# Optimization experiments

Hardware: AMD Instinct MI355X
Metric: run time of the kernel (lower is better)

The kernel has to match this reference:

```python
import jax, jax.numpy as jnp
import numpy as np

B, N, C = 1, 2048, 1024
H, D = 16, 64          # num_heads, head_dim
S = 8                  # number of frames; tokens per frame = N // S
NEG_INF = jnp.float32(-1e30)  # stand-in for -inf, numerically safe under jit


def setup_inputs() -> dict:
    key = jax.random.key(0)
    ks = jax.random.split(key, 8)
    x = jax.random.normal(ks[0], (B, N, C), dtype=jnp.float32)
    # tokens grouped contiguously by frame (sorted frame ids)
    frame_ids = jnp.repeat(jnp.arange(S, dtype=jnp.int32), N // S)
    is_hub = jax.random.bernoulli(ks[1], 0.05, (N,))
    adj = jax.random.bernoulli(ks[2], 0.25, (S, S))
    adj = adj.at[jnp.arange(S), jnp.arange(S)].set(True)  # frames always see self
    frame_bias = jax.random.normal(ks[3], (S, S), dtype=jnp.float32) * 0.1
    Wqkv = jax.random.normal(ks[4], (C, 3 * C), dtype=jnp.float32) * 0.02
    bqkv = jnp.zeros((3 * C,), dtype=jnp.float32)
    Wproj = jax.random.normal(ks[5], (C, C), dtype=jnp.float32) * 0.02
    bproj = jnp.zeros((C,), dtype=jnp.float32)
    return {"x": x, "frame_ids": frame_ids, "is_hub": is_hub, "adj": adj,
            "frame_bias": frame_bias, "Wqkv": Wqkv, "bqkv": bqkv,
            "Wproj": Wproj, "bproj": bproj}


def reference(x, frame_ids, is_hub, adj, frame_bias, Wqkv, bqkv, Wproj, bproj):
    # qkv projection: (B,N,3C) -> (3,B,H,N,D)
    qkv = (x @ Wqkv + bqkv).reshape(B, N, 3, H, D).transpose(2, 0, 3, 1, 4)
    q, k, v = qkv[0], qkv[1], qkv[2]

    # flex_attention: scores scaled by 1/sqrt(D) BEFORE score_mod
    scores = jnp.einsum("bhnd,bhmd->bhnm", q, k) * (D ** -0.5)

    # score_mod, vectorized over all (qi,kj) pairs:
    fi = frame_ids                                   # (N,)
    allow = adj[fi][:, fi]                           # (N,N) frame adjacency per token pair
    diff_frame = fi[:, None] != fi[None, :]
    hub_block = diff_frame & (is_hub[:, None] | is_hub[None, :])
    allow = allow & ~hub_block                       # mask_hub_tokens=True
    bias = frame_bias[fi][:, fi]                     # soft_mask=True: add frame-level bias

    scores = jnp.where(allow, scores + bias, NEG_INF)  # broadcast over (b,h)
    attn = jax.nn.softmax(scores, axis=-1)
    out = jnp.einsum("bhnm,bhmd->bhnd", attn, v)
    out = out.transpose(0, 2, 1, 3).reshape(B, N, C)
    return out @ Wproj + bproj
```

## Files before the change

### kernel.cpp

```cpp
#include <hip/hip_runtime.h>

#define NTOK 2048
#define CDIM 1024
#define NHEAD 16
#define HDIM 64
#define NFRM 8
#define FTOK 256

typedef unsigned short ushort;
typedef __attribute__((ext_vector_type(8))) short short8;
typedef __attribute__((ext_vector_type(8))) ushort ushort8;
typedef __attribute__((ext_vector_type(4))) ushort ushort4v;
typedef __attribute__((ext_vector_type(4))) float floatx4;

__device__ __forceinline__ ushort f2bf(float f) {
    unsigned int u = __float_as_uint(f);
    return (ushort)((u + 0x7fffu + ((u >> 16) & 1u)) >> 16);
}

__device__ __forceinline__ void gload_lds16(const void* g, void* l) {
    __builtin_amdgcn_global_load_lds(
        (const __attribute__((address_space(1))) unsigned int*)(uintptr_t)g,
        (__attribute__((address_space(3))) unsigned int*)(unsigned int)(uintptr_t)l,
        16, 0, 0);
}

__global__ __launch_bounds__(256)
void convx_kernel(const float* __restrict__ x, ushort* __restrict__ xb, int n4)
{
    int i = blockIdx.x * 256 + threadIdx.x;
    if (i < n4) {
        float4 f = ((const float4*)x)[i];
        ushort4v o = { f2bf(f.x), f2bf(f.y), f2bf(f.z), f2bf(f.w) };
        ((ushort4v*)xb)[i] = o;
    }
}

__global__ __launch_bounds__(256)
void wtrans_kernel(const float* __restrict__ W, ushort* __restrict__ WT, int K, int N)
{
    __shared__ ushort LT[64][72];
    const int t = threadIdx.x;
    const int k0 = blockIdx.y * 64, n0 = blockIdx.x * 64;
    const int kr = t >> 4, nc = t & 15;
#pragma unroll
    for (int i = 0; i < 4; ++i) {
        int k = kr + i * 16;
        float4 w4 = *(const float4*)(W + (size_t)(k0 + k) * N + n0 + nc * 4);
        LT[nc*4+0][k] = f2bf(w4.x);
        LT[nc*4+1][k] = f2bf(w4.y);
        LT[nc*4+2][k] = f2bf(w4.z);
        LT[nc*4+3][k] = f2bf(w4.w);
    }
    __syncthreads();
    const int n = t >> 2;
#pragma unroll
    for (int half = 0; half < 2; ++half) {
        int kc = (t & 3) + 4 * half;
        ushort8 v = *(const ushort8*)&LT[n][kc * 8];
        *(ushort8*)(WT + (size_t)(n0 + n) * K + k0 + kc * 8) = v;
    }
}

__global__ __launch_bounds__(256)
void vtrans_kernel(const ushort* __restrict__ v, ushort* __restrict__ vT)
{
    __shared__ ushort LT[64][72];
    const int t = threadIdx.x, h = blockIdx.y, n0 = blockIdx.x * 64;
    {
        const int tok = t >> 2;
#pragma unroll
        for (int half = 0; half < 2; ++half) {
            int dc = (t & 3) + 4 * half;
            ushort8 v8 = *(const ushort8*)(v + ((size_t)h * NTOK + n0 + tok) * HDIM + dc * 8);
#pragma unroll
            for (int j = 0; j < 8; ++j) LT[dc*8 + j][tok] = v8[j];
        }
    }
    __syncthreads();
    {
        const int d = t >> 2;
#pragma unroll
        for (int half = 0; half < 2; ++half) {
            int tc = (t & 3) + 4 * half;
            ushort8 o8 = *(const ushort8*)&LT[d][tc * 8];
            *(ushort8*)(vT + ((size_t)h * HDIM + d) * NTOK + n0 + tc * 8) = o8;
        }
    }
}

__global__ __launch_bounds__(256)
void gemm_bt_kernel(const ushort* __restrict__ A, const ushort* __restrict__ BT,
                    const float* __restrict__ bias, void* __restrict__ out,
                    int M, int N, int K, int mode)
{
    __shared__ ushort As[2][128 * 32];
    __shared__ ushort Bs[2][128 * 32];

    const int t = threadIdx.x;
    const int wave = t >> 6, lane = t & 63;
    const int quad = lane >> 4, l15 = lane & 15;
    const int row0 = blockIdx.y * 128, col0 = blockIdx.x * 128;
    const int wm = (wave >> 1) * 64, wn = (wave & 1) * 64;

    const int sr = lane >> 2;
    const int sc = (lane & 3) * 8;
    const int r0 = wave * 32;

    floatx4 acc[4][4];
#pragma unroll
    for (int i = 0; i < 4; ++i)
#pragma unroll
        for (int j = 0; j < 4; ++j) acc[i][j] = (floatx4){0.f, 0.f, 0.f, 0.f};

    gload_lds16(A  + (size_t)(row0 + r0      + sr) * K + sc, &As[0][ r0       * 32]);
    gload_lds16(A  + (size_t)(row0 + r0 + 16 + sr) * K + sc, &As[0][(r0 + 16) * 32]);
    gload_lds16(BT + (size_t)(col0 + r0      + sr) * K + sc, &Bs[0][ r0       * 32]);
    gload_lds16(BT + (size_t)(col0 + r0 + 16 + sr) * K + sc, &Bs[0][(r0 + 16) * 32]);

    const int nk = K >> 5;
    for (int ki = 0; ki < nk; ++ki) {
        __syncthreads();
        if (ki + 1 < nk) {
            const int kn = (ki + 1) << 5;
            const int b = (ki + 1) & 1;
            gload_lds16(A  + (size_t)(row0 + r0      + sr) * K + kn + sc, &As[b][ r0       * 32]);
            gload_lds16(A  + (size_t)(row0 + r0 + 16 + sr) * K + kn + sc, &As[b][(r0 + 16) * 32]);
            gload_lds16(BT + (size_t)(col0 + r0      + sr) * K + kn + sc, &Bs[b][ r0       * 32]);
            gload_lds16(BT + (size_t)(col0 + r0 + 16 + sr) * K + kn + sc, &Bs[b][(r0 + 16) * 32]);
        }
        const ushort* as = As[ki & 1];
        const ushort* bs = Bs[ki & 1];

        short8 af[4], bfr[4];
#pragma unroll
        for (int i = 0; i < 4; ++i)
            af[i] = *(const short8*)&as[(wm + i * 16 + l15) * 32 + quad * 8];
#pragma unroll
        for (int j = 0; j < 4; ++j)
            bfr[j] = *(const short8*)&bs[(wn + j * 16 + l15) * 32 + quad * 8];
#pragma unroll
        for (int i = 0; i < 4; ++i)
#pragma unroll
            for (int j = 0; j < 4; ++j)
                acc[i][j] = __builtin_amdgcn_mfma_f32_16x16x32_bf16(af[i], bfr[j], acc[i][j], 0, 0, 0);
    }

    if (mode == 0) {
        float* outf = (float*)out;
#pragma unroll
        for (int j = 0; j < 4; ++j) {
            int col = col0 + wn + j * 16 + l15;
            float bb = bias[col];
#pragma unroll
            for (int i = 0; i < 4; ++i) {
                int rowb = row0 + wm + i * 16 + quad * 4;
#pragma unroll
                for (int r = 0; r < 4; ++r)
                    outf[(size_t)(rowb + r) * N + col] = acc[i][j][r] + bb;
            }
        }
    } else {
        ushort* outb = (ushort*)out;
#pragma unroll
        for (int j = 0; j < 4; ++j) {
            int col = col0 + wn + j * 16 + l15;
            float bb = bias[col];
            int part = col >> 10, hh = (col >> 6) & 15, d = col & 63;
            ushort* dst = outb + ((size_t)(part * NHEAD + hh) * NTOK) * HDIM + d;
#pragma unroll
            for (int i = 0; i < 4; ++i) {
                int rowb = row0 + wm + i * 16 + quad * 4;
#pragma unroll
                for (int r = 0; r < 4; ++r)
                    dst[(size_t)(rowb + r) * HDIM] = f2bf(acc[i][j][r] + bb);
            }
        }
    }
}

__global__ __launch_bounds__(256)
void attn_mfma_kernel(const ushort* __restrict__ qkvb,
                      const ushort* __restrict__ vTb,
                      const int* __restrict__ frame_ids,
                      const int* __restrict__ is_hub,
                      const int* __restrict__ adj,
                      const float* __restrict__ frame_bias,
                      ushort* __restrict__ attnb)
{
    __shared__ ushort Qs[64 * 64];
    __shared__ ushort Ks[2][64 * 64];
    __shared__ ushort VTs[2][64 * 64];
    __shared__ ushort Ps[4][16 * 72];

    const int t = threadIdx.x;
    const int wave = t >> 6, lane = t & 63;
    const int quad = lane >> 4, l15 = lane & 15;
    const int h = blockIdx.y, q0 = blockIdx.x * 64;

    const ushort* Qg = qkvb + ((size_t)h * NTOK) * HDIM;
    const ushort* Kg = qkvb + ((size_t)(NHEAD + h) * NTOK) * HDIM;
    const ushort* Vg = vTb + ((size_t)h * HDIM) * NTOK;

    const int sr = lane >> 3;
    const int sc = (lane & 7) * 8;
    const int r0s = wave * 16;

    const int fq = frame_ids[q0];
    unsigned vpack = 0; int nv = 0;
#pragma unroll
    for (int f = 0; f < NFRM; ++f)
        if (adj[fq * NFRM + f]) { vpack |= (unsigned)f << (3 * nv); ++nv; }
    const int ntot = nv * 4;

    {
        gload_lds16(Qg + (size_t)(q0 + r0s     + sr) * HDIM + sc, &Qs[ r0s      * 64]);
        gload_lds16(Qg + (size_t)(q0 + r0s + 8 + sr) * HDIM + sc, &Qs[(r0s + 8) * 64]);
        const int k0 = (int)(vpack & 7u) * FTOK;
        gload_lds16(Kg + (size_t)(k0 + r0s     + sr) * HDIM + sc, &Ks[0][ r0s      * 64]);
        gload_lds16(Kg + (size_t)(k0 + r0s + 8 + sr) * HDIM + sc, &Ks[0][(r0s + 8) * 64]);
        gload_lds16(Vg + (size_t)(r0s     + sr) * NTOK + k0 + sc, &VTs[0][ r0s      * 64]);
        gload_lds16(Vg + (size_t)(r0s + 8 + sr) * NTOK + k0 + sc, &VTs[0][(r0s + 8) * 64]);
    }

    int qh[4];
#pragma unroll
    for (int r = 0; r < 4; ++r) qh[r] = is_hub[q0 + wave * 16 + quad * 4 + r];

    float mcur[4], lcur[4];
    floatx4 oacc[4];
#pragma unroll
    for (int r = 0; r < 4; ++r) { mcur[r] = -3.0e38f; lcur[r] = 0.0f; }
#pragma unroll
    for (int dt = 0; dt < 4; ++dt) oacc[dt] = (floatx4){0.f, 0.f, 0.f, 0.f};

    short8 aq0, aq1;

    for (int vt = 0; vt < ntot; ++vt) {
        const int fj = (int)((vpack >> (3 * (vt >> 2))) & 7u);
        const int k0 = fj * FTOK + (vt & 3) * 64;

        __syncthreads();

        if (vt == 0) {
            aq0 = *(const short8*)&Qs[(wave * 16 + l15) * 64 + quad * 8];
            aq1 = *(const short8*)&Qs[(wave * 16 + l15) * 64 + 32 + quad * 8];
        }
        if (vt + 1 < ntot) {
            const int fn = (int)((vpack >> (3 * ((vt + 1) >> 2))) & 7u);
            const int kn = fn * FTOK + ((vt + 1) & 3) * 64;
            const int b = (vt + 1) & 1;
            gload_lds16(Kg + (size_t)(kn + r0s     + sr) * HDIM + sc, &Ks[b][ r0s      * 64]);
            gload_lds16(Kg + (size_t)(kn + r0s + 8 + sr) * HDIM + sc, &Ks[b][(r0s + 8) * 64]);
            gload_lds16(Vg + (size_t)(r0s     + sr) * NTOK + kn + sc, &VTs[b][ r0s      * 64]);
            gload_lds16(Vg + (size_t)(r0s + 8 + sr) * NTOK + kn + sc, &VTs[b][(r0s + 8) * 64]);
        }

        int kh[4];
#pragma unroll
        for (int nt = 0; nt < 4; ++nt) kh[nt] = is_hub[k0 + nt * 16 + l15];
        const float fb = frame_bias[fq * NFRM + fj];
        const bool same = (fj == fq);

        const ushort* ks = Ks[vt & 1];
        const ushort* vs = VTs[vt & 1];

        floatx4 s[4];
#pragma unroll
        for (int nt = 0; nt < 4; ++nt) s[nt] = (floatx4){0.f, 0.f, 0.f, 0.f};
#pragma unroll
        for (int nt = 0; nt < 4; ++nt) {
            short8 bk0 = *(const short8*)&ks[(nt * 16 + l15) * 64 + quad * 8];
            short8 bk1 = *(const short8*)&ks[(nt * 16 + l15) * 64 + 32 + quad * 8];
            s[nt] = __builtin_amdgcn_mfma_f32_16x16x32_bf16(aq0, bk0, s[nt], 0, 0, 0);
            s[nt] = __builtin_amdgcn_mfma_f32_16x16x32_bf16(aq1, bk1, s[nt], 0, 0, 0);
        }

        float alpha[4];
#pragma unroll
        for (int r = 0; r < 4; ++r) {
            float sv[4];
#pragma unroll
            for (int nt = 0; nt < 4; ++nt) {
                bool allow = same || ((qh[r] == 0) && (kh[nt] == 0));
                sv[nt] = allow ? fmaf(s[nt][r], 0.125f, fb) : -1.0e30f;
            }
            float rm = fmaxf(fmaxf(sv[0], sv[1]), fmaxf(sv[2], sv[3]));
            rm = fmaxf(rm, __shfl_xor(rm, 1));
            rm = fmaxf(rm, __shfl_xor(rm, 2));
            rm = fmaxf(rm, __shfl_xor(rm, 4));
            rm = fmaxf(rm, __shfl_xor(rm, 8));
            float mnew = fmaxf(mcur[r], rm);
            float a = __expf(mcur[r] - mnew);
            float p[4], sum = 0.0f;
#pragma unroll
            for (int nt = 0; nt < 4; ++nt) { p[nt] = __expf(sv[nt] - mnew); sum += p[nt]; }
            sum += __shfl_xor(sum, 1);
            sum += __shfl_xor(sum, 2);
            sum += __shfl_xor(sum, 4);
            sum += __shfl_xor(sum, 8);
            lcur[r] = lcur[r] * a + sum;
            mcur[r] = mnew;
            alpha[r] = a;
#pragma unroll
            for (int nt = 0; nt < 4; ++nt)
                Ps[wave][(quad * 4 + r) * 72 + nt * 16 + l15] = f2bf(p[nt]);
        }
#pragma unroll
        for (int dt = 0; dt < 4; ++dt)
#pragma unroll
            for (int r = 0; r < 4; ++r) oacc[dt][r] *= alpha[r];

        short8 ap0 = *(const short8*)&Ps[wave][l15 * 72 + quad * 8];
        short8 ap1 = *(const short8*)&Ps[wave][l15 * 72 + 32 + quad * 8];
#pragma unroll
        for (int dt = 0; dt < 4; ++dt) {
            short8 bv0 = *(const short8*)&vs[(dt * 16 + l15) * 64 + quad * 8];
            short8 bv1 = *(const short8*)&vs[(dt * 16 + l15) * 64 + 32 + quad * 8];
            oacc[dt] = __builtin_amdgcn_mfma_f32_16x16x32_bf16(ap0, bv0, oacc[dt], 0, 0, 0);
            oacc[dt] = __builtin_amdgcn_mfma_f32_16x16x32_bf16(ap1, bv1, oacc[dt], 0, 0, 0);
        }
    }

#pragma unroll
    for (int dt = 0; dt < 4; ++dt) {
        int col = h * HDIM + dt * 16 + l15;
#pragma unroll
        for (int r = 0; r < 4; ++r) {
            int row = q0 + wave * 16 + quad * 4 + r;
            attnb[(size_t)row * CDIM + col] = f2bf(oacc[dt][r] / lcur[r]);
        }
    }
}

extern "C" void kernel_launch(void* const* d_in, const int* in_sizes, int n_in,
                              void* d_out, int out_size, void* d_ws, size_t ws_size,
                              hipStream_t stream)
{
    const float* x          = (const float*)d_in[0];
    const int*   frame_ids  = (const int*)d_in[1];
    const int*   is_hub     = (const int*)d_in[2];
    const int*   adj        = (const int*)d_in[3];
    const float* frame_bias = (const float*)d_in[4];
    const float* Wqkv       = (const float*)d_in[5];
    const float* bqkv       = (const float*)d_in[6];
    const float* Wproj      = (const float*)d_in[7];
    const float* bproj      = (const float*)d_in[8];
    float* out = (float*)d_out;

    ushort* xb     = (ushort*)d_ws;
    ushort* wqkvT  = xb     + 2097152;
    ushort* wprojT = wqkvT  + 3145728;
    ushort* qkvb   = wprojT + 1048576;
    ushort* vTb    = qkvb   + 6291456;
    ushort* attnb  = vTb    + 2097152;

    dim3 blk(256);

    convx_kernel<<<dim3((NTOK * CDIM / 4 + 255) / 256), blk, 0, stream>>>(x, xb, NTOK * CDIM / 4);
    wtrans_kernel<<<dim3(3 * CDIM / 64, CDIM / 64), blk, 0, stream>>>(Wqkv, wqkvT, CDIM, 3 * CDIM);
    wtrans_kernel<<<dim3(CDIM / 64, CDIM / 64), blk, 0, stream>>>(Wproj, wprojT, CDIM, CDIM);

    gemm_bt_kernel<<<dim3(3 * CDIM / 128, NTOK / 128), blk, 0, stream>>>(
        xb, wqkvT, bqkv, qkvb, NTOK, 3 * CDIM, CDIM, 1);

    vtrans_kernel<<<dim3(NTOK / 64, NHEAD), blk, 0, stream>>>(
        qkvb + (size_t)2 * NHEAD * NTOK * HDIM, vTb);

    attn_mfma_kernel<<<dim3(NTOK / 64, NHEAD), blk, 0, stream>>>(
        qkvb, vTb, frame_ids, is_hub, adj, frame_bias, attnb);

    gemm_bt_kernel<<<dim3(CDIM / 128, NTOK / 128), blk, 0, stream>>>(
        attnb, wprojT, bproj, out, NTOK, CDIM, CDIM, 0);
}
```

Measured before the change: 173.7 us.

## Merge prep kernels and make attention one wave per block without LDS staging

The x conversion and both weight transposes are combined into one prep kernel launch, which removes two launches. The attention kernel now runs one 64-thread wave per 16-query block. It reads K and V^T fragments straight from global memory into registers, with no LDS double buffering and no block barriers. This drops the sync overhead and raises the block count, but K/V reuse across the four waves that used to share a tile now has to come from cache, so global traffic may rise.

New measurement: 190.2 us. 9.5% more time.

```diff
diff --git a/kernel.cpp b/kernel.cpp
--- a/kernel.cpp
+++ b/kernel.cpp
@@ -26,22 +26,27 @@
 }
 
 __global__ __launch_bounds__(256)
-void convx_kernel(const float* __restrict__ x, ushort* __restrict__ xb, int n4)
-{
-    int i = blockIdx.x * 256 + threadIdx.x;
-    if (i < n4) {
+void prep_kernel(const float* __restrict__ x, ushort* __restrict__ xb,
+                 const float* __restrict__ Wqkv, ushort* __restrict__ wqkvT,
+                 const float* __restrict__ Wproj, ushort* __restrict__ wprojT)
+{
+    __shared__ ushort LT[64][72];
+    const int b = blockIdx.x, t = threadIdx.x;
+
+    if (b < 2048) {
+        int i = b * 256 + t;
         float4 f = ((const float4*)x)[i];
         ushort4v o = { f2bf(f.x), f2bf(f.y), f2bf(f.z), f2bf(f.w) };
         ((ushort4v*)xb)[i] = o;
-    }
-}
-
-__global__ __launch_bounds__(256)
-void wtrans_kernel(const float* __restrict__ W, ushort* __restrict__ WT, int K, int N)
-{
-    __shared__ ushort LT[64][72];
-    const int t = threadIdx.x;
-    const int k0 = blockIdx.y * 64, n0 = blockIdx.x * 64;
+        return;
+    }
+
+    const float* W; ushort* WT; int K, N, n0, k0;
+    if (b < 2816) { int idx = b - 2048; W = Wqkv;  WT = wqkvT;  K = 1024; N = 3072;
+                    n0 = (idx % 48) * 64; k0 = (idx / 48) * 64; }
+    else          { int idx = b - 2816; W = Wproj; WT = wprojT; K = 1024; N = 1024;
+                    n0 = (idx & 15) * 64; k0 = (idx >> 4) * 64; }
+
     const int kr = t >> 4, nc = t & 15;
 #pragma unroll
     for (int i = 0; i < 4; ++i) {
@@ -179,8 +184,8 @@
     }
 }
 
-__global__ __launch_bounds__(256)
-void attn_mfma_kernel(const ushort* __restrict__ qkvb,
+__global__ __launch_bounds__(64)
+void attn_wave_kernel(const ushort* __restrict__ qkvb,
                       const ushort* __restrict__ vTb,
                       const int* __restrict__ frame_ids,
                       const int* __restrict__ is_hub,
@@ -188,23 +193,18 @@
                       const float* __restrict__ frame_bias,
                       ushort* __restrict__ attnb)
 {
-    __shared__ ushort Qs[64 * 64];
-    __shared__ ushort Ks[2][64 * 64];
-    __shared__ ushort VTs[2][64 * 64];
-    __shared__ ushort Ps[4][16 * 72];
-
-    const int t = threadIdx.x;
-    const int wave = t >> 6, lane = t & 63;
+    __shared__ ushort Ps[16 * 72];
+
+    const int lane = threadIdx.x;
     const int quad = lane >> 4, l15 = lane & 15;
-    const int h = blockIdx.y, q0 = blockIdx.x * 64;
+    const int h = blockIdx.y, q0 = blockIdx.x * 16;
 
     const ushort* Qg = qkvb + ((size_t)h * NTOK) * HDIM;
     const ushort* Kg = qkvb + ((size_t)(NHEAD + h) * NTOK) * HDIM;
     const ushort* Vg = vTb + ((size_t)h * HDIM) * NTOK;
 
-    const int sr = lane >> 3;
-    const int sc = (lane & 7) * 8;
-    const int r0s = wave * 16;
+    short8 aq0 = *(const short8*)(Qg + (size_t)(q0 + l15) * HDIM + quad * 8);
+    short8 aq1 = *(const short8*)(Qg + (size_t)(q0 + l15) * HDIM + 32 + quad * 8);
 
     const int fq = frame_ids[q0];
     unsigned vpack = 0; int nv = 0;
@@ -213,19 +213,9 @@
         if (adj[fq * NFRM + f]) { vpack |= (unsigned)f << (3 * nv); ++nv; }
     const int ntot = nv * 4;
 
-    {
-        gload_lds16(Qg + (size_t)(q0 + r0s     + sr) * HDIM + sc, &Qs[ r0s      * 64]);
-        gload_lds16(Qg + (size_t)(q0 + r0s + 8 + sr) * HDIM + sc, &Qs[(r0s + 8) * 64]);
-        const int k0 = (int)(vpack & 7u) * FTOK;
-        gload_lds16(Kg + (size_t)(k0 + r0s     + sr) * HDIM + sc, &Ks[0][ r0s      * 64]);
-        gload_lds16(Kg + (size_t)(k0 + r0s + 8 + sr) * HDIM + sc, &Ks[0][(r0s + 8) * 64]);
-        gload_lds16(Vg + (size_t)(r0s     + sr) * NTOK + k0 + sc, &VTs[0][ r0s      * 64]);
-        gload_lds16(Vg + (size_t)(r0s + 8 + sr) * NTOK + k0 + sc, &VTs[0][(r0s + 8) * 64]);
-    }
-
     int qh[4];
 #pragma unroll
-    for (int r = 0; r < 4; ++r) qh[r] = is_hub[q0 + wave * 16 + quad * 4 + r];
+    for (int r = 0; r < 4; ++r) qh[r] = is_hub[q0 + quad * 4 + r];
 
     float mcur[4], lcur[4];
     floatx4 oacc[4];
@@ -233,45 +223,30 @@
     for (int r = 0; r < 4; ++r) { mcur[r] = -3.0e38f; lcur[r] = 0.0f; }
 #pragma unroll
     for (int dt = 0; dt < 4; ++dt) oacc[dt] = (floatx4){0.f, 0.f, 0.f, 0.f};
-
-    short8 aq0, aq1;
 
     for (int vt = 0; vt < ntot; ++vt) {
         const int fj = (int)((vpack >> (3 * (vt >> 2))) & 7u);
         const int k0 = fj * FTOK + (vt & 3) * 64;
-
-        __syncthreads();
-
-        if (vt == 0) {
-            aq0 = *(const short8*)&Qs[(wave * 16 + l15) * 64 + quad * 8];
-            aq1 = *(const short8*)&Qs[(wave * 16 + l15) * 64 + 32 + quad * 8];
-        }
-        if (vt + 1 < ntot) {
-            const int fn = (int)((vpack >> (3 * ((vt + 1) >> 2))) & 7u);
-            const int kn = fn * FTOK + ((vt + 1) & 3) * 64;
-            const int b = (vt + 1) & 1;
-            gload_lds16(Kg + (size_t)(kn + r0s     + sr) * HDIM + sc, &Ks[b][ r0s      * 64]);
-            gload_lds16(Kg + (size_t)(kn + r0s + 8 + sr) * HDIM + sc, &Ks[b][(r0s + 8) * 64]);
-            gload_lds16(Vg + (size_t)(r0s     + sr) * NTOK + kn + sc, &VTs[b][ r0s      * 64]);
-            gload_lds16(Vg + (size_t)(r0s + 8 + sr) * NTOK + kn + sc, &VTs[b][(r0s + 8) * 64]);
-        }
-
-        int kh[4];
-#pragma unroll
-        for (int nt = 0; nt < 4; ++nt) kh[nt] = is_hub[k0 + nt * 16 + l15];
         const float fb = frame_bias[fq * NFRM + fj];
         const bool same = (fj == fq);
 
-        const ushort* ks = Ks[vt & 1];
-        const ushort* vs = VTs[vt & 1];
+        short8 bv[4][2];
+#pragma unroll
+        for (int dt = 0; dt < 4; ++dt) {
+            bv[dt][0] = *(const short8*)(Vg + (size_t)(dt * 16 + l15) * NTOK + k0 + quad * 8);
+            bv[dt][1] = *(const short8*)(Vg + (size_t)(dt * 16 + l15) * NTOK + k0 + 32 + quad * 8);
+        }
+        int kh[4];
+#pragma unroll
+        for (int nt = 0; nt < 4; ++nt) kh[nt] = is_hub[k0 + nt * 16 + l15];
 
         floatx4 s[4];
 #pragma unroll
         for (int nt = 0; nt < 4; ++nt) s[nt] = (floatx4){0.f, 0.f, 0.f, 0.f};
 #pragma unroll
         for (int nt = 0; nt < 4; ++nt) {
-            short8 bk0 = *(const short8*)&ks[(nt * 16 + l15) * 64 + quad * 8];
-            short8 bk1 = *(const short8*)&ks[(nt * 16 + l15) * 64 + 32 + quad * 8];
+            short8 bk0 = *(const short8*)(Kg + (size_t)(k0 + nt * 16 + l15) * HDIM + quad * 8);
+            short8 bk1 = *(const short8*)(Kg + (size_t)(k0 + nt * 16 + l15) * HDIM + 32 + quad * 8);
             s[nt] = __builtin_amdgcn_mfma_f32_16x16x32_bf16(aq0, bk0, s[nt], 0, 0, 0);
             s[nt] = __builtin_amdgcn_mfma_f32_16x16x32_bf16(aq1, bk1, s[nt], 0, 0, 0);
         }
@@ -304,21 +279,19 @@
             alpha[r] = a;
 #pragma unroll
             for (int nt = 0; nt < 4; ++nt)
-                Ps[wave][(quad * 4 + r) * 72 + nt * 16 + l15] = f2bf(p[nt]);
+                Ps[(quad * 4 + r) * 72 + nt * 16 + l15] = f2bf(p[nt]);
         }
 #pragma unroll
         for (int dt = 0; dt < 4; ++dt)
 #pragma unroll
             for (int r = 0; r < 4; ++r) oacc[dt][r] *= alpha[r];
 
-        short8 ap0 = *(const short8*)&Ps[wave][l15 * 72 + quad * 8];
-        short8 ap1 = *(const short8*)&Ps[wave][l15 * 72 + 32 + quad * 8];
+        short8 ap0 = *(const short8*)&Ps[l15 * 72 + quad * 8];
+        short8 ap1 = *(const short8*)&Ps[l15 * 72 + 32 + quad * 8];
 #pragma unroll
         for (int dt = 0; dt < 4; ++dt) {
-            short8 bv0 = *(const short8*)&vs[(dt * 16 + l15) * 64 + quad * 8];
-            short8 bv1 = *(const short8*)&vs[(dt * 16 + l15) * 64 + 32 + quad * 8];
-            oacc[dt] = __builtin_amdgcn_mfma_f32_16x16x32_bf16(ap0, bv0, oacc[dt], 0, 0, 0);
-            oacc[dt] = __builtin_amdgcn_mfma_f32_16x16x32_bf16(ap1, bv1, oacc[dt], 0, 0, 0);
+            oacc[dt] = __builtin_amdgcn_mfma_f32_16x16x32_bf16(ap0, bv[dt][0], oacc[dt], 0, 0, 0);
+            oacc[dt] = __builtin_amdgcn_mfma_f32_16x16x32_bf16(ap1, bv[dt][1], oacc[dt], 0, 0, 0);
         }
     }
 
@@ -327,7 +300,7 @@
         int col = h * HDIM + dt * 16 + l15;
 #pragma unroll
         for (int r = 0; r < 4; ++r) {
-            int row = q0 + wave * 16 + quad * 4 + r;
+            int row = q0 + quad * 4 + r;
             attnb[(size_t)row * CDIM + col] = f2bf(oacc[dt][r] / lcur[r]);
         }
     }
@@ -355,21 +328,17 @@
     ushort* vTb    = qkvb   + 6291456;
     ushort* attnb  = vTb    + 2097152;
 
-    dim3 blk(256);
-
-    convx_kernel<<<dim3((NTOK * CDIM / 4 + 255) / 256), blk, 0, stream>>>(x, xb, NTOK * CDIM / 4);
-    wtrans_kernel<<<dim3(3 * CDIM / 64, CDIM / 64), blk, 0, stream>>>(Wqkv, wqkvT, CDIM, 3 * CDIM);
-    wtrans_kernel<<<dim3(CDIM / 64, CDIM / 64), blk, 0, stream>>>(Wproj, wprojT, CDIM, CDIM);
-
-    gemm_bt_kernel<<<dim3(3 * CDIM / 128, NTOK / 128), blk, 0, stream>>>(
+    prep_kernel<<<dim3(3072), dim3(256), 0, stream>>>(x, xb, Wqkv, wqkvT, Wproj, wprojT);
+
+    gemm_bt_kernel<<<dim3(3 * CDIM / 128, NTOK / 128), dim3(256), 0, stream>>>(
         xb, wqkvT, bqkv, qkvb, NTOK, 3 * CDIM, CDIM, 1);
 
-    vtrans_kernel<<<dim3(NTOK / 64, NHEAD), blk, 0, stream>>>(
+    vtrans_kernel<<<dim3(NTOK / 64, NHEAD), dim3(256), 0, stream>>>(
         qkvb + (size_t)2 * NHEAD * NTOK * HDIM, vTb);
 
-    attn_mfma_kernel<<<dim3(NTOK / 64, NHEAD), blk, 0, stream>>>(
+    attn_wave_kernel<<<dim3(NTOK / 16, NHEAD), dim3(64), 0, stream>>>(
         qkvb, vTb, frame_ids, is_hub, adj, frame_bias, attnb);
 
-    gemm_bt_kernel<<<dim3(CDIM / 128, NTOK / 128), blk, 0, stream>>>(
+    gemm_bt_kernel<<<dim3(CDIM / 128, NTOK / 128), dim3(256), 0, stream>>>(
         attnb, wprojT, bproj, out, NTOK, CDIM, CDIM, 0);
 }
```
